# Kernel tuning notes

Hardware: AMD Instinct MI355X
Metric: run time of the kernel (lower is better)

## Reference

```python
import jax, jax.numpy as jnp
import numpy as np

DIM = 2048
N_HEADS = 16
N_KV = 8
NUM_REP = N_HEADS // N_KV  # 2
HEAD_DIM = DIM // N_HEADS // 2  # 64
EPS = 1e-5
THETA = 10000.0
B, S = 2, 2048


def setup_inputs() -> dict:
    key = jax.random.key(0)
    ks = jax.random.split(key, 12)
    x = jax.random.normal(ks[0], (B, S, DIM), dtype=jnp.float32)
    wq = jax.random.normal(ks[1], (DIM, DIM), dtype=jnp.float32) * 0.02
    wk = jax.random.normal(ks[2], (DIM, DIM // NUM_REP), dtype=jnp.float32) * 0.02
    wv = jax.random.normal(ks[3], (DIM, DIM // NUM_REP), dtype=jnp.float32) * 0.02
    wo = jax.random.normal(ks[4], (DIM, DIM), dtype=jnp.float32) * 0.02
    lambda_q1 = jax.random.normal(ks[5], (HEAD_DIM,), dtype=jnp.float32) * 0.1
    lambda_k1 = jax.random.normal(ks[6], (HEAD_DIM,), dtype=jnp.float32) * 0.1
    lambda_q2 = jax.random.normal(ks[7], (HEAD_DIM,), dtype=jnp.float32) * 0.1
    lambda_k2 = jax.random.normal(ks[8], (HEAD_DIM,), dtype=jnp.float32) * 0.1
    lambda_init = jnp.array([0.8], dtype=jnp.float32)
    subln_w = jnp.ones((2 * HEAD_DIM,), dtype=jnp.float32)
    # rope tables: precompute_freqs_cis(dim=2*HEAD_DIM) then sliced to first HEAD_DIM//2 freqs
    exps = jnp.arange(0, HEAD_DIM, 2, dtype=jnp.float32) / (2.0 * HEAD_DIM)
    freqs = THETA ** (-exps)  # [HEAD_DIM//2]
    ang = jnp.arange(S, dtype=jnp.float32)[:, None] * freqs[None, :]  # [S, HEAD_DIM//2]
    return {
        "x": x, "wq": wq, "wk": wk, "wv": wv, "wo": wo,
        "lambda_q1": lambda_q1, "lambda_k1": lambda_k1,
        "lambda_q2": lambda_q2, "lambda_k2": lambda_k2,
        "lambda_init": lambda_init, "subln_w": subln_w,
        "freqs_cos": jnp.cos(ang), "freqs_sin": jnp.sin(ang),
    }


def _rope(t, cos, sin):
    # t: [B,S,H,hd]; cos/sin: [S, hd//2]; complex-pair rotation on (even, odd)
    e, o = t[..., 0::2], t[..., 1::2]
    c = cos[None, :, None, :]
    s = sin[None, :, None, :]
    return jnp.stack([e * c - o * s, e * s + o * c], axis=-1).reshape(t.shape)


def _repeat_kv_buggy(t, n_rep):
    # faithful to source: t is [B, n_kv, S, hd]; unsqueeze at dim 3 then reshape,
    # which flattens (n_kv, S, rep) -> (n_kv*rep, S)
    b, n_kv, slen, hd = t.shape
    exp = jnp.broadcast_to(t[:, :, :, None, :], (b, n_kv, slen, n_rep, hd))
    return exp.reshape(b, n_kv * n_rep, slen, hd)


def _attn(q, k, v, scale):
    # q,k: [B,H,S,hd]; v: [B,H,S,2hd]
    scores = jnp.einsum('bhqd,bhkd->bhqk', q, k) * scale
    p = jax.nn.softmax(scores, axis=-1)
    return jnp.einsum('bhqk,bhkd->bhqd', p, v)


def reference(x, wq, wk, wv, wo, lambda_q1, lambda_k1, lambda_q2, lambda_k2,
              lambda_init, subln_w, freqs_cos, freqs_sin):
    bsz, seqlen, _ = x.shape
    scale = HEAD_DIM ** -0.5
    q = (x @ wq).reshape(bsz, seqlen, 2 * N_HEADS, HEAD_DIM)
    k = (x @ wk).reshape(bsz, seqlen, 2 * N_KV, HEAD_DIM)
    v = (x @ wv).reshape(bsz, seqlen, N_KV, 2 * HEAD_DIM)
    q = _rope(q, freqs_cos, freqs_sin)
    k = _rope(k, freqs_cos, freqs_sin)
    q = q.reshape(bsz, seqlen, N_HEADS, 2, HEAD_DIM)
    k = k.reshape(bsz, seqlen, N_KV, 2, HEAD_DIM)
    q1 = q[:, :, :, 0].transpose(0, 2, 1, 3)  # [B,H,S,hd]
    q2 = q[:, :, :, 1].transpose(0, 2, 1, 3)
    k1 = _repeat_kv_buggy(k[:, :, :, 0].transpose(0, 2, 1, 3), NUM_REP)
    k2 = _repeat_kv_buggy(k[:, :, :, 1].transpose(0, 2, 1, 3), NUM_REP)
    vr = _repeat_kv_buggy(v.transpose(0, 2, 1, 3), NUM_REP)  # [B,H,S,2hd]
    attn1 = _attn(q1, k1, vr, scale)
    attn2 = _attn(q2, k2, vr, scale)
    lambda_1 = jnp.exp(jnp.sum(lambda_q1 * lambda_k1))
    lambda_2 = jnp.exp(jnp.sum(lambda_q2 * lambda_k2))
    lambda_full = lambda_1 - lambda_2 + lambda_init[0]
    attn = attn1 - lambda_full * attn2  # [B,H,S,2hd]
    # sub-layer RMSNorm over 2*HEAD_DIM
    rms = jax.lax.rsqrt(jnp.mean(attn * attn, axis=-1, keepdims=True) + EPS)
    attn = attn * rms * subln_w
    attn = attn * (1.0 - lambda_init[0])
    attn = attn.transpose(0, 2, 1, 3).reshape(bsz, seqlen, N_HEADS * 2 * HEAD_DIM)
    return attn @ wo
```

## Files before the change

### kernel.cpp

```cpp
#include <hip/hip_runtime.h>
#include <stdint.h>

typedef unsigned short u16;
typedef __attribute__((ext_vector_type(8))) short bf16x8v;
typedef __attribute__((ext_vector_type(4))) float f32x4;

#define DIM   2048
#define NH    16
#define NKV   8
#define HD    64
#define B_    2
#define S_    2048
#define ROWS  (B_*S_)
#define NQKV  4096
#define EPS_   1e-5f
#define SCALE_ 0.125f

__device__ __forceinline__ u16 bfbits(float f) {
  union { float f; unsigned int u; } a; a.f = f;
  unsigned int u = a.u;
  return (u16)((u + 0x7FFFu + ((u >> 16) & 1u)) >> 16);
}

__device__ __forceinline__ f32x4 mfma16(bf16x8v a, bf16x8v b, f32x4 c) {
  return __builtin_amdgcn_mfma_f32_16x16x32_bf16(a, b, c, 0, 0, 0);
}

__device__ __forceinline__ void gload_lds16(const void* g, void* l) {
  __builtin_amdgcn_global_load_lds(
      (const __attribute__((address_space(1))) unsigned int*)g,
      (__attribute__((address_space(3))) unsigned int*)l, 16, 0, 0);
}

__global__ void cast_f32_bf16(const float* __restrict__ src, u16* __restrict__ dst, int n4) {
  int i = blockIdx.x * 256 + threadIdx.x;
  if (i >= n4) return;
  float4 v = ((const float4*)src)[i];
  ushort4 o; o.x = bfbits(v.x); o.y = bfbits(v.y); o.z = bfbits(v.z); o.w = bfbits(v.w);
  ((ushort4*)dst)[i] = o;
}

__global__ void transpose_cast(const float* __restrict__ src, u16* __restrict__ dst, int R, int C) {
  __shared__ float t[32][33];
  int c0 = blockIdx.x * 32, r0 = blockIdx.y * 32;
  int x = threadIdx.x, y = threadIdx.y;
#pragma unroll
  for (int i = 0; i < 4; ++i) t[y + 8*i][x] = src[(size_t)(r0 + y + 8*i) * C + c0 + x];
  __syncthreads();
#pragma unroll
  for (int i = 0; i < 4; ++i) dst[(size_t)(c0 + y + 8*i) * R + r0 + x] = bfbits(t[x][y + 8*i]);
}

__global__ void v_transpose(const float* __restrict__ qkv, u16* __restrict__ Vt) {
  __shared__ float t[32][33];
  int z = blockIdx.z;
  int b = z >> 3, kv = z & 7;
  int s0 = blockIdx.x * 32, d0 = blockIdx.y * 32;
  int x = threadIdx.x, y = threadIdx.y;
  const float* src = qkv + (size_t)b * S_ * NQKV + 3072 + kv * 128;
#pragma unroll
  for (int i = 0; i < 4; ++i) t[y + 8*i][x] = src[(size_t)(s0 + y + 8*i) * NQKV + d0 + x];
  __syncthreads();
  u16* dst = Vt + ((size_t)(b * NKV + kv) * 128) * S_;
#pragma unroll
  for (int i = 0; i < 4; ++i) dst[(size_t)(d0 + y + 8*i) * S_ + s0 + x] = bfbits(t[x][y + 8*i]);
}

__global__ void rope_kernel(const float* __restrict__ qkv, const float* __restrict__ fc,
                            const float* __restrict__ fs, u16* __restrict__ D1, u16* __restrict__ D2,
                            int hshift, int coloff) {
  int p = blockIdx.x * 256 + threadIdx.x;
  int i = p & 31;
  int hh = (p >> 5) & ((1 << hshift) - 1);
  int row = p >> (5 + hshift);
  int s = row & (S_ - 1);
  int b = row >> 11;
  const float* src = qkv + (size_t)row * NQKV + coloff + hh * HD + 2 * i;
  float e = src[0], o = src[1];
  float c = fc[s * 32 + i], sn = fs[s * 32 + i];
  float r0 = e * c - o * sn, r1 = e * sn + o * c;
  u16* dst = (hh & 1) ? D2 : D1;
  int nh = 1 << (hshift - 1);
  size_t offo = (((size_t)b * nh + (hh >> 1)) * S_ + s) * HD + 2 * i;
  unsigned int packed = (unsigned int)bfbits(r0) | ((unsigned int)bfbits(r1) << 16);
  *(unsigned int*)(dst + offo) = packed;
}

__global__ void lambda_kernel(const float* lq1, const float* lk1, const float* lq2,
                              const float* lk2, const float* li, float* scal) {
  int t = threadIdx.x;
  float p1 = lq1[t] * lk1[t];
  float p2 = lq2[t] * lk2[t];
#pragma unroll
  for (int off = 32; off > 0; off >>= 1) { p1 += __shfl_xor(p1, off); p2 += __shfl_xor(p2, off); }
  if (t == 0) {
    scal[0] = __expf(p1) - __expf(p2) + li[0];
    scal[1] = 1.0f - li[0];
  }
}

__global__ __launch_bounds__(256) void gemm_bt(const u16* __restrict__ A, const u16* __restrict__ Bt,
                                               float* __restrict__ C, int M, int N, int K) {
  __shared__ u16 As[128 * 32];
  __shared__ u16 Bs[128 * 32];
  const int tid = threadIdx.x;
  const int wave = tid >> 6, lane = tid & 63;
  const int lr = lane & 15, lk = (lane >> 4) * 8;
  const size_t row0 = (size_t)blockIdx.y * 128, col0 = (size_t)blockIdx.x * 128;
  const int wr = (wave >> 1) * 64, wc = (wave & 1) * 64;
  f32x4 acc[4][4] = {};
  for (int kt = 0; kt < K; kt += 32) {
#pragma unroll
    for (int i = 0; i < 2; ++i) {
      int c = i * 256 + tid;
      int r = c >> 2, c8 = (c & 3) * 8;
      gload_lds16(A  + (row0 + r) * (size_t)K + kt + c8, (char*)As + (i * 256 + wave * 64) * 16);
      gload_lds16(Bt + (col0 + r) * (size_t)K + kt + c8, (char*)Bs + (i * 256 + wave * 64) * 16);
    }
    __syncthreads();
    bf16x8v af[4], bv[4];
#pragma unroll
    for (int m = 0; m < 4; ++m) af[m] = *(const bf16x8v*)(As + (wr + m * 16 + lr) * 32 + lk);
#pragma unroll
    for (int n = 0; n < 4; ++n) bv[n] = *(const bf16x8v*)(Bs + (wc + n * 16 + lr) * 32 + lk);
#pragma unroll
    for (int m = 0; m < 4; ++m)
#pragma unroll
      for (int n = 0; n < 4; ++n) acc[m][n] = mfma16(af[m], bv[n], acc[m][n]);
    __syncthreads();
  }
  const int crow = (lane >> 4) * 4;
#pragma unroll
  for (int m = 0; m < 4; ++m)
#pragma unroll
    for (int n = 0; n < 4; ++n) {
      float* cp = C + (row0 + wr + m * 16 + crow) * (size_t)N + col0 + wc + n * 16 + lr;
#pragma unroll
      for (int j = 0; j < 4; ++j) cp[(size_t)j * N] = acc[m][n][j];
    }
}

__device__ __forceinline__ void attn_step(const u16* Ks, const u16* Vts, u16* Pw,
                                          const bf16x8v* qf, float* m, float* l, f32x4* O,
                                          int lane) {
  const int lr = lane & 15, cq = lane >> 4, crow = cq * 4;
  f32x4 s[4] = {};
#pragma unroll
  for (int kf = 0; kf < 4; ++kf) {
    const int row = kf * 16 + lr, sw = row & 7;
    s[kf] = mfma16(qf[0], *(const bf16x8v*)(Ks + row * 64 + ((cq ^ sw) * 8)), s[kf]);
    s[kf] = mfma16(qf[1], *(const bf16x8v*)(Ks + row * 64 + (((cq + 4) ^ sw) * 8)), s[kf]);
  }
  float pm[4] = {-1e30f, -1e30f, -1e30f, -1e30f};
#pragma unroll
  for (int kf = 0; kf < 4; ++kf)
#pragma unroll
    for (int j = 0; j < 4; ++j) {
      float sv = s[kf][j] * SCALE_;
      s[kf][j] = sv;
      pm[j] = fmaxf(pm[j], sv);
    }
#pragma unroll
  for (int off = 1; off < 16; off <<= 1)
#pragma unroll
    for (int j = 0; j < 4; ++j) pm[j] = fmaxf(pm[j], __shfl_xor(pm[j], off));
  float al[4], ps[4];
#pragma unroll
  for (int j = 0; j < 4; ++j) {
    float mn = fmaxf(m[j], pm[j]);
    al[j] = __expf(m[j] - mn);
    m[j] = mn;
    ps[j] = 0.f;
  }
#pragma unroll
  for (int kf = 0; kf < 4; ++kf)
#pragma unroll
    for (int j = 0; j < 4; ++j) {
      float p = __expf(s[kf][j] - m[j]);
      s[kf][j] = p;
      ps[j] += p;
    }
#pragma unroll
  for (int off = 1; off < 16; off <<= 1)
#pragma unroll
    for (int j = 0; j < 4; ++j) ps[j] += __shfl_xor(ps[j], off);
#pragma unroll
  for (int j = 0; j < 4; ++j) l[j] = l[j] * al[j] + ps[j];
#pragma unroll
  for (int f = 0; f < 8; ++f)
#pragma unroll
    for (int j = 0; j < 4; ++j) O[f][j] *= al[j];
#pragma unroll
  for (int kf = 0; kf < 4; ++kf) {
    const int ch = kf * 2 + (lr >> 3), cl = lr & 7;
#pragma unroll
    for (int j = 0; j < 4; ++j) {
      const int row = crow + j;
      Pw[row * 64 + ((ch ^ (row & 7)) * 8) + cl] = bfbits(s[kf][j]);
    }
  }
#pragma unroll
  for (int kst = 0; kst < 2; ++kst) {
    bf16x8v pf = *(const bf16x8v*)(Pw + lr * 64 + (((kst * 4 + cq) ^ (lr & 7)) * 8));
#pragma unroll
    for (int f = 0; f < 8; ++f) {
      const int row = f * 16 + lr;
      bf16x8v vf = *(const bf16x8v*)(Vts + row * 64 + (((kst * 4 + cq) ^ (row & 7)) * 8));
      O[f] = mfma16(pf, vf, O[f]);
    }
  }
}

__global__ __launch_bounds__(256) void attn_kernel(
    const u16* __restrict__ Q1, const u16* __restrict__ Q2,
    const u16* __restrict__ K1g, const u16* __restrict__ K2g,
    const u16* __restrict__ Vt, const float* __restrict__ scal,
    const float* __restrict__ subw, u16* __restrict__ attnb) {
  __shared__ u16 K1s[64 * 64];
  __shared__ u16 K2s[64 * 64];
  __shared__ u16 Vts[128 * 64];
  __shared__ u16 Ps[4][16 * 64];
  const int qb = blockIdx.x, h = blockIdx.y, b = blockIdx.z;
  const int tid = threadIdx.x;
  const int wave = tid >> 6, lane = tid & 63;
  const int lr = lane & 15, lkq = (lane >> 4) * 8;
  const int crow = (lane >> 4) * 4;
  const int kv = h >> 1;
  const int keybase = (h & 1) * 1024;

  const int srow = qb * 64 + wave * 16 + lr;
  const u16* q1p = Q1 + (((size_t)b * NH + h) * S_ + srow) * HD + lkq;
  const u16* q2p = Q2 + (((size_t)b * NH + h) * S_ + srow) * HD + lkq;
  bf16x8v q1f[2], q2f[2];
  q1f[0] = *(const bf16x8v*)(q1p);       q1f[1] = *(const bf16x8v*)(q1p + 32);
  q2f[0] = *(const bf16x8v*)(q2p);       q2f[1] = *(const bf16x8v*)(q2p + 32);

  f32x4 O1[8] = {}, O2[8] = {};
  float m1[4], l1[4], m2[4], l2[4];
#pragma unroll
  for (int j = 0; j < 4; ++j) { m1[j] = -1e30f; l1[j] = 0.f; m2[j] = -1e30f; l2[j] = 0.f; }

  const u16* k1b = K1g + ((size_t)b * NKV + kv) * S_ * HD;
  const u16* k2b = K2g + ((size_t)b * NKV + kv) * S_ * HD;
  const u16* vb  = Vt  + ((size_t)b * NKV + kv) * 128 * S_;

  for (int ck = 0; ck < 16; ++ck) {
    const int key0 = keybase + ck * 64;
#pragma unroll
    for (int i = 0; i < 2; ++i) {
      int n = i * 256 + tid;
      int r = n >> 3, cl = (n & 7) ^ (r & 7);
      gload_lds16(k1b + (size_t)(key0 + r) * HD + cl * 8, (char*)K1s + (i * 256 + wave * 64) * 16);
      gload_lds16(k2b + (size_t)(key0 + r) * HD + cl * 8, (char*)K2s + (i * 256 + wave * 64) * 16);
    }
#pragma unroll
    for (int i = 0; i < 4; ++i) {
      int n = i * 256 + tid;
      int r = n >> 3, cl = (n & 7) ^ (r & 7);
      gload_lds16(vb + (size_t)r * S_ + key0 + cl * 8, (char*)Vts + (i * 256 + wave * 64) * 16);
    }
    __syncthreads();
    attn_step(K1s, Vts, Ps[wave], q1f, m1, l1, O1, lane);
    attn_step(K2s, Vts, Ps[wave], q2f, m2, l2, O2, lane);
    __syncthreads();
  }

  const float lam = scal[0], ofac = scal[1];
  float ssq[4] = {0.f, 0.f, 0.f, 0.f};
#pragma unroll
  for (int f = 0; f < 8; ++f)
#pragma unroll
    for (int j = 0; j < 4; ++j) {
      float cv = O1[f][j] / l1[j] - lam * (O2[f][j] / l2[j]);
      O1[f][j] = cv;
      ssq[j] += cv * cv;
    }
#pragma unroll
  for (int off = 1; off < 16; off <<= 1)
#pragma unroll
    for (int j = 0; j < 4; ++j) ssq[j] += __shfl_xor(ssq[j], off);
  float rs[4];
#pragma unroll
  for (int j = 0; j < 4; ++j) rs[j] = rsqrtf(ssq[j] * (1.f / 128.f) + EPS_) * ofac;
  const size_t rowb = (size_t)b * S_ + qb * 64 + wave * 16 + crow;
#pragma unroll
  for (int f = 0; f < 8; ++f) {
    float sw = subw[f * 16 + lr];
#pragma unroll
    for (int j = 0; j < 4; ++j)
      attnb[(rowb + j) * DIM + h * 128 + f * 16 + lr] = bfbits(O1[f][j] * rs[j] * sw);
  }
}

extern "C" void kernel_launch(void* const* d_in, const int* in_sizes, int n_in,
                              void* d_out, int out_size, void* d_ws, size_t ws_size,
                              hipStream_t stream) {
  const float* x   = (const float*)d_in[0];
  const float* wq  = (const float*)d_in[1];
  const float* wk  = (const float*)d_in[2];
  const float* wv  = (const float*)d_in[3];
  const float* wo  = (const float*)d_in[4];
  const float* lq1 = (const float*)d_in[5];
  const float* lk1 = (const float*)d_in[6];
  const float* lq2 = (const float*)d_in[7];
  const float* lk2 = (const float*)d_in[8];
  const float* li  = (const float*)d_in[9];
  const float* subw= (const float*)d_in[10];
  const float* fc  = (const float*)d_in[11];
  const float* fs  = (const float*)d_in[12];
  float* out = (float*)d_out;

  char* ws = (char*)d_ws;
  size_t off = 0;
  auto alloc = [&](size_t bytes) { char* p = ws + off; off += (bytes + 255) & ~(size_t)255; return p; };
  u16*   xb    = (u16*)alloc((size_t)ROWS * DIM * 2);
  u16*   wqkvT = (u16*)alloc((size_t)NQKV * DIM * 2);
  u16*   woT   = (u16*)alloc((size_t)DIM * DIM * 2);
  float* qkv   = (float*)alloc((size_t)ROWS * NQKV * 4);
  u16*   Q1    = (u16*)alloc((size_t)B_ * NH * S_ * HD * 2);
  u16*   Q2    = (u16*)alloc((size_t)B_ * NH * S_ * HD * 2);
  u16*   K1    = (u16*)alloc((size_t)B_ * NKV * S_ * HD * 2);
  u16*   K2    = (u16*)alloc((size_t)B_ * NKV * S_ * HD * 2);
  u16*   Vt    = (u16*)alloc((size_t)B_ * NKV * 128 * S_ * 2);
  u16*   attnb = (u16*)alloc((size_t)ROWS * DIM * 2);
  float* scal  = (float*)alloc(256);

  cast_f32_bf16<<<ROWS * DIM / 4 / 256, 256, 0, stream>>>(x, xb, ROWS * DIM / 4);
  transpose_cast<<<dim3(64, 64), dim3(32, 8), 0, stream>>>(wq, wqkvT, DIM, DIM);
  transpose_cast<<<dim3(32, 64), dim3(32, 8), 0, stream>>>(wk, wqkvT + (size_t)2048 * DIM, DIM, 1024);
  transpose_cast<<<dim3(32, 64), dim3(32, 8), 0, stream>>>(wv, wqkvT + (size_t)3072 * DIM, DIM, 1024);
  transpose_cast<<<dim3(64, 64), dim3(32, 8), 0, stream>>>(wo, woT, DIM, DIM);

  gemm_bt<<<dim3(NQKV / 128, ROWS / 128), 256, 0, stream>>>(xb, wqkvT, qkv, ROWS, NQKV, DIM);

  rope_kernel<<<ROWS * 32 * 32 / 256, 256, 0, stream>>>(qkv, fc, fs, Q1, Q2, 5, 0);
  rope_kernel<<<ROWS * 16 * 32 / 256, 256, 0, stream>>>(qkv, fc, fs, K1, K2, 4, 2048);
  v_transpose<<<dim3(64, 4, 16), dim3(32, 8), 0, stream>>>(qkv, Vt);
  lambda_kernel<<<1, 64, 0, stream>>>(lq1, lk1, lq2, lk2, li, scal);

  attn_kernel<<<dim3(32, NH, B_), 256, 0, stream>>>(Q1, Q2, K1, K2, Vt, scal, subw, attnb);

  gemm_bt<<<dim3(DIM / 128, ROWS / 128), 256, 0, stream>>>(attnb, woT, out, ROWS, DIM, DIM);
}
```

Baseline: 539.3 us.

## Double-buffer attention K/V tiles, defer softmax rescale, raise MFMA wave priority

Splits the K1/K2/V LDS tiles into two buffers so the next key tile's global-to-LDS loads are issued before computing on the current tile, overlapping memory latency with compute and removing one barrier per iteration. Skips the running-max update and the rescaling of the output accumulators when every row's new max stays within a threshold of the old one (lazy rescale). Raises wave priority around the MFMA sections. Doubling LDS use may reduce occupancy, and the single barrier relies on the async LDS loads being complete when it is reached, which is not obviously guaranteed.

Result: slower. 559.7 us (+3.8%).

```diff
diff --git a/kernel.cpp b/kernel.cpp
--- a/kernel.cpp
+++ b/kernel.cpp
@@ -15,6 +15,7 @@
 #define NQKV  4096
 #define EPS_   1e-5f
 #define SCALE_ 0.125f
+#define RESCALE_THR 8.0f
 
 __device__ __forceinline__ u16 bfbits(float f) {
   union { float f; unsigned int u; } a; a.f = f;
@@ -145,12 +146,14 @@
                                           int lane) {
   const int lr = lane & 15, cq = lane >> 4, crow = cq * 4;
   f32x4 s[4] = {};
+  __builtin_amdgcn_s_setprio(1);
 #pragma unroll
   for (int kf = 0; kf < 4; ++kf) {
     const int row = kf * 16 + lr, sw = row & 7;
     s[kf] = mfma16(qf[0], *(const bf16x8v*)(Ks + row * 64 + ((cq ^ sw) * 8)), s[kf]);
     s[kf] = mfma16(qf[1], *(const bf16x8v*)(Ks + row * 64 + (((cq + 4) ^ sw) * 8)), s[kf]);
   }
+  __builtin_amdgcn_s_setprio(0);
   float pm[4] = {-1e30f, -1e30f, -1e30f, -1e30f};
 #pragma unroll
   for (int kf = 0; kf < 4; ++kf)
@@ -164,12 +167,19 @@
   for (int off = 1; off < 16; off <<= 1)
 #pragma unroll
     for (int j = 0; j < 4; ++j) pm[j] = fmaxf(pm[j], __shfl_xor(pm[j], off));
+  bool okl = true;
+#pragma unroll
+  for (int j = 0; j < 4; ++j) okl = okl && (pm[j] <= m[j] + RESCALE_THR);
+  const bool defer = (__all(okl ? 1 : 0) != 0);
   float al[4], ps[4];
 #pragma unroll
   for (int j = 0; j < 4; ++j) {
-    float mn = fmaxf(m[j], pm[j]);
-    al[j] = __expf(m[j] - mn);
-    m[j] = mn;
+    if (defer) { al[j] = 1.f; }
+    else {
+      float mn = fmaxf(m[j], pm[j]);
+      al[j] = __expf(m[j] - mn);
+      m[j] = mn;
+    }
     ps[j] = 0.f;
   }
 #pragma unroll
@@ -186,10 +196,12 @@
     for (int j = 0; j < 4; ++j) ps[j] += __shfl_xor(ps[j], off);
 #pragma unroll
   for (int j = 0; j < 4; ++j) l[j] = l[j] * al[j] + ps[j];
-#pragma unroll
-  for (int f = 0; f < 8; ++f)
-#pragma unroll
-    for (int j = 0; j < 4; ++j) O[f][j] *= al[j];
+  if (!defer) {
+#pragma unroll
+    for (int f = 0; f < 8; ++f)
+#pragma unroll
+      for (int j = 0; j < 4; ++j) O[f][j] *= al[j];
+  }
 #pragma unroll
   for (int kf = 0; kf < 4; ++kf) {
     const int ch = kf * 2 + (lr >> 3), cl = lr & 7;
@@ -199,6 +211,7 @@
       Pw[row * 64 + ((ch ^ (row & 7)) * 8) + cl] = bfbits(s[kf][j]);
     }
   }
+  __builtin_amdgcn_s_setprio(1);
 #pragma unroll
   for (int kst = 0; kst < 2; ++kst) {
     bf16x8v pf = *(const bf16x8v*)(Pw + lr * 64 + (((kst * 4 + cq) ^ (lr & 7)) * 8));
@@ -208,6 +221,25 @@
       bf16x8v vf = *(const bf16x8v*)(Vts + row * 64 + (((kst * 4 + cq) ^ (row & 7)) * 8));
       O[f] = mfma16(pf, vf, O[f]);
     }
+  }
+  __builtin_amdgcn_s_setprio(0);
+}
+
+__device__ __forceinline__ void stage_tile(const u16* k1b, const u16* k2b, const u16* vb,
+                                           int key0, u16* K1d, u16* K2d, u16* Vd,
+                                           int tid, int wave) {
+#pragma unroll
+  for (int i = 0; i < 2; ++i) {
+    int n = i * 256 + tid;
+    int r = n >> 3, cl = (n & 7) ^ (r & 7);
+    gload_lds16(k1b + (size_t)(key0 + r) * HD + cl * 8, (char*)K1d + (i * 256 + wave * 64) * 16);
+    gload_lds16(k2b + (size_t)(key0 + r) * HD + cl * 8, (char*)K2d + (i * 256 + wave * 64) * 16);
+  }
+#pragma unroll
+  for (int i = 0; i < 4; ++i) {
+    int n = i * 256 + tid;
+    int r = n >> 3, cl = (n & 7) ^ (r & 7);
+    gload_lds16(vb + (size_t)r * S_ + key0 + cl * 8, (char*)Vd + (i * 256 + wave * 64) * 16);
   }
 }
 
@@ -216,9 +248,9 @@
     const u16* __restrict__ K1g, const u16* __restrict__ K2g,
     const u16* __restrict__ Vt, const float* __restrict__ scal,
     const float* __restrict__ subw, u16* __restrict__ attnb) {
-  __shared__ u16 K1s[64 * 64];
-  __shared__ u16 K2s[64 * 64];
-  __shared__ u16 Vts[128 * 64];
+  __shared__ u16 K1s[2][64 * 64];
+  __shared__ u16 K2s[2][64 * 64];
+  __shared__ u16 Vts[2][128 * 64];
   __shared__ u16 Ps[4][16 * 64];
   const int qb = blockIdx.x, h = blockIdx.y, b = blockIdx.z;
   const int tid = threadIdx.x;
@@ -244,25 +276,15 @@
   const u16* k2b = K2g + ((size_t)b * NKV + kv) * S_ * HD;
   const u16* vb  = Vt  + ((size_t)b * NKV + kv) * 128 * S_;
 
+  stage_tile(k1b, k2b, vb, keybase, K1s[0], K2s[0], Vts[0], tid, wave);
   for (int ck = 0; ck < 16; ++ck) {
-    const int key0 = keybase + ck * 64;
-#pragma unroll
-    for (int i = 0; i < 2; ++i) {
-      int n = i * 256 + tid;
-      int r = n >> 3, cl = (n & 7) ^ (r & 7);
-      gload_lds16(k1b + (size_t)(key0 + r) * HD + cl * 8, (char*)K1s + (i * 256 + wave * 64) * 16);
-      gload_lds16(k2b + (size_t)(key0 + r) * HD + cl * 8, (char*)K2s + (i * 256 + wave * 64) * 16);
-    }
-#pragma unroll
-    for (int i = 0; i < 4; ++i) {
-      int n = i * 256 + tid;
-      int r = n >> 3, cl = (n & 7) ^ (r & 7);
-      gload_lds16(vb + (size_t)r * S_ + key0 + cl * 8, (char*)Vts + (i * 256 + wave * 64) * 16);
-    }
+    const int cur = ck & 1;
     __syncthreads();
-    attn_step(K1s, Vts, Ps[wave], q1f, m1, l1, O1, lane);
-    attn_step(K2s, Vts, Ps[wave], q2f, m2, l2, O2, lane);
-    __syncthreads();
+    if (ck < 15)
+      stage_tile(k1b, k2b, vb, keybase + (ck + 1) * 64,
+                 K1s[cur ^ 1], K2s[cur ^ 1], Vts[cur ^ 1], tid, wave);
+    attn_step(K1s[cur], Vts[cur], Ps[wave], q1f, m1, l1, O1, lane);
+    attn_step(K2s[cur], Vts[cur], Ps[wave], q2f, m2, l2, O2, lane);
   }
 
   const float lam = scal[0], ofac = scal[1];
```
